# Kernel optimization log

Measured on AMD Instinct MI355X. Metric: run time of the kernel, lower is better.

Reference implementation:

```python
import jax, jax.numpy as jnp
import numpy as np

B, S, H = 16, 2048, 1024

def setup_inputs() -> dict:
    key = jax.random.key(0)
    ks = jax.random.split(key, 6)
    return {
        "h": jax.random.normal(ks[0], (1, B, H), jnp.float32),
        "c": jax.random.normal(ks[1], (1, B, H), jnp.float32),
        "encoder_outputs": jax.random.normal(ks[2], (B, S, H), jnp.float32),
        "attn_W": jax.random.normal(ks[3], (H, 2 * H), jnp.float32) * 0.02,
        "attn_b": jax.random.normal(ks[4], (H,), jnp.float32) * 0.02,
        "v_W": jax.random.normal(ks[5], (1, H), jnp.float32) * 0.02,
    }

def reference(h, c, encoder_outputs, attn_W, attn_b, v_W):
    # h: (1,B,H) -> (B,1,H); a: (B,S,H)
    a = encoder_outputs
    hq = jnp.transpose(h, (1, 0, 2))  # (B,1,H)
    # cat((s, a), -1) @ attn_W.T == s @ Wh.T + a @ Wa.T (avoids (B,S,2H) buffer)
    Wh, Wa = attn_W[:, :H], attn_W[:, H:]
    energy = jax.nn.relu(
        jnp.einsum("bqh,oh->bqo", hq, Wh)          # (B,1,H), broadcast over S
        + jnp.einsum("bsh,oh->bso", a, Wa)
        + attn_b
    )  # (B,S,H)
    scores = jnp.einsum("bsh,h->bs", energy, v_W[0])  # (B,S)
    attn_weights = jax.nn.softmax(scores, axis=1)      # (B,S)
    context = jnp.einsum("bs,bsh->bh", attn_weights, a)[:, None, :]  # (B,1,H)
    return context, attn_weights
```

## Files before the change

kernel.cpp:

```cpp
#include <hip/hip_runtime.h>
#include <hip/hip_bf16.h>


typedef __bf16 bf16x8 __attribute__((ext_vector_type(8)));
typedef float floatx4 __attribute__((ext_vector_type(4)));

#define BB 16
#define SS 2048
#define HH 1024
#define MM (BB * SS)

#define GLB(p) ((const __attribute__((address_space(1))) void*)(p))
#define LDSP(p) ((__attribute__((address_space(3))) void*)(p))

__device__ inline ushort f2bf(float x) {
    uint32_t u = __builtin_bit_cast(uint32_t, x);
    u += 0x7FFFu + ((u >> 16) & 1u);
    return (ushort)(u >> 16);
}

__global__ __launch_bounds__(256) void prep_all_kernel(
    const float* __restrict__ h, const float* __restrict__ W,
    const float* __restrict__ bias,
    float* __restrict__ projh, __bf16* __restrict__ Wb,
    float* __restrict__ sp0, float* __restrict__ ctx)
{
    int bid = blockIdx.x;
    int tid = threadIdx.x;
    if (bid < 256) {
        int b = bid >> 4;
        int oc = bid & 15;
        __shared__ float hrow[HH];
        *(float4*)&hrow[tid * 4] = *(const float4*)(h + (size_t)b * HH + tid * 4);
        __syncthreads();
        int ol = tid >> 2;
        int kq = tid & 3;
        int o = oc * 64 + ol;
        const float* wr = W + (size_t)o * (2 * HH) + kq * 256;
        const float* hb = hrow + kq * 256;
        float sum = 0.f;
        for (int k = 0; k < 256; k += 4) {
            float4 wv = *(const float4*)(wr + k);
            sum += hb[k] * wv.x + hb[k + 1] * wv.y + hb[k + 2] * wv.z + hb[k + 3] * wv.w;
        }
        sum += __shfl_xor(sum, 1);
        sum += __shfl_xor(sum, 2);
        if (kq == 0) projh[b * HH + o] = sum + bias[o];
    } else if (bid < 320) {
        int cb = bid - 256;
#pragma unroll
        for (int j = 0; j < 8; j++) {
            int g = cb * 2048 + tid + j * 256;
            int o = g >> 7;
            int k = (g & 127) * 8;
            const float* s = W + (size_t)o * (2 * HH) + HH + k;
            float4 x = *(const float4*)(s);
            float4 y = *(const float4*)(s + 4);
            union { ushort u[8]; uint4 v; } p;
            p.u[0] = f2bf(x.x); p.u[1] = f2bf(x.y); p.u[2] = f2bf(x.z); p.u[3] = f2bf(x.w);
            p.u[4] = f2bf(y.x); p.u[5] = f2bf(y.y); p.u[6] = f2bf(y.z); p.u[7] = f2bf(y.w);
            *(uint4*)(Wb + (size_t)o * HH + k) = p.v;
        }
    } else {
        int zb = bid - 320;
        float4 z = make_float4(0.f, 0.f, 0.f, 0.f);
        float* sp = sp0 + zb * 2048 + tid * 8;
        *(float4*)(sp) = z;
        *(float4*)(sp + 4) = z;
        *(float4*)(ctx + zb * 1024 + tid * 4) = z;
    }
}

__global__ __launch_bounds__(512, 2) void gemm_scores_kernel(
    const float* __restrict__ Af,
    const __bf16* __restrict__ Wb,
    const float* __restrict__ projh,
    const float* __restrict__ vW,
    float* __restrict__ scores_part)
{
    __shared__ __align__(16) char smem_raw[147456];
    __bf16* sB = (__bf16*)(smem_raw + 98304);

    const int bid = blockIdx.x;
    const int m0 = (((bid >> 5) << 3) + (bid & 7)) * 256;
    const int nq = (bid >> 3) & 3;
    const int n0 = nq * 256;
    const int bidx = m0 >> 11;

    const int tid = threadIdx.x;
    const int lane = tid & 63;
    const int wave = tid >> 6;
    const int wm = (wave & 1) * 128;
    const int wn = (wave >> 1) * 64;
    const int quad = lane >> 4;
    const int l16 = lane & 15;

    floatx4 acc[8][4];
    const floatx4 z = {0.f, 0.f, 0.f, 0.f};
#pragma unroll
    for (int i = 0; i < 8; i++)
#pragma unroll
        for (int j = 0; j < 4; j++) acc[i][j] = z;

    const int rb = lane >> 3;
    const int cchunk = ((lane & 7) ^ rb) * 4;
    const float* gAq0 = Af + (size_t)(m0 +   0 + wave * 8 + rb) * HH + cchunk;
    const float* gAq1 = Af + (size_t)(m0 +  64 + wave * 8 + rb) * HH + cchunk;
    const float* gAq2 = Af + (size_t)(m0 + 128 + wave * 8 + rb) * HH + cchunk;
    const float* gAq3 = Af + (size_t)(m0 + 192 + wave * 8 + rb) * HH + cchunk;

    const int su = tid >> 3;
    const int sj = (tid & 7) ^ (su & 7);
    const int g_row = su * 2 + (sj >> 2);
    const int g_col = (sj & 3) * 8;
    const __bf16* gB0 = Wb + (size_t)(n0 + g_row) * HH + g_col;
    const __bf16* gB1 = gB0 + (size_t)128 * HH;

    const int axL = (quad * 32) ^ ((l16 & 7) << 4);
    const int axH = axL ^ 16;
    int arow[8];
#pragma unroll
    for (int i = 0; i < 8; i++) arow[i] = (wm + i * 16 + l16) * 128;

    int boff[4];
#pragma unroll
    for (int j = 0; j < 4; j++) {
        int frow = wn + j * 16 + l16;
        int r7 = frow & 127;
        int u2 = r7 >> 1;
        int cc = u2 * 8 + (((((r7 & 1) << 2) | quad)) ^ (u2 & 7));
        boff[j] = (frow >> 7) * 4096 + cc * 8;
    }

#define STAGE_A(S, KF)                                                                       \
    {                                                                                        \
        char* dA_ = smem_raw + (S) * 32768 + wave * 1024;                                    \
        __builtin_amdgcn_global_load_lds(GLB(gAq0 + (KF)), LDSP(dA_), 16, 0, 0);             \
        __builtin_amdgcn_global_load_lds(GLB(gAq1 + (KF)), LDSP(dA_ + 8192), 16, 0, 0);      \
        __builtin_amdgcn_global_load_lds(GLB(gAq2 + (KF)), LDSP(dA_ + 16384), 16, 0, 0);     \
        __builtin_amdgcn_global_load_lds(GLB(gAq3 + (KF)), LDSP(dA_ + 24576), 16, 0, 0);     \
    }
#define STAGE_B(S, KF)                                                                       \
    {                                                                                        \
        __bf16* dB_ = sB + (S) * 8192 + wave * 512;                                          \
        __builtin_amdgcn_global_load_lds(GLB(gB0 + (KF)), LDSP(dB_), 16, 0, 0);              \
        __builtin_amdgcn_global_load_lds(GLB(gB1 + (KF)), LDSP(dB_ + 4096), 16, 0, 0);       \
    }
#define CVT8(dst, L, H)                                                     \
    {                                                                       \
        dst[0] = (__bf16)(L).x; dst[1] = (__bf16)(L).y;                     \
        dst[2] = (__bf16)(L).z; dst[3] = (__bf16)(L).w;                     \
        dst[4] = (__bf16)(H).x; dst[5] = (__bf16)(H).y;                     \
        dst[6] = (__bf16)(H).z; dst[7] = (__bf16)(H).w;                     \
    }
#define MFMA_LO                                                                            \
    _Pragma("unroll") for (int i_ = 0; i_ < 4; i_++)                                       \
        _Pragma("unroll") for (int j_ = 0; j_ < 4; j_++)                                   \
            acc[i_][j_] = __builtin_amdgcn_mfma_f32_16x16x32_bf16(af[i_], bfr[j_], acc[i_][j_], 0, 0, 0);
#define MFMA_HI                                                                            \
    _Pragma("unroll") for (int i_ = 0; i_ < 4; i_++)                                       \
        _Pragma("unroll") for (int j_ = 0; j_ < 4; j_++)                                   \
            acc[i_ + 4][j_] = __builtin_amdgcn_mfma_f32_16x16x32_bf16(af2[i_], bfr[j_], acc[i_ + 4][j_], 0, 0, 0);
#define BAR __builtin_amdgcn_s_barrier()
#define LGKM0 asm volatile("s_waitcnt lgkmcnt(0)" ::: "memory")
#define VM6 asm volatile("s_waitcnt vmcnt(6)" ::: "memory")
#define VM0 asm volatile("s_waitcnt vmcnt(0)" ::: "memory")
#define NOPW
#define PRIO1 __builtin_amdgcn_s_setprio(1)
#define PRIO0 __builtin_amdgcn_s_setprio(0)

#define KTILE(SC, SN, KF, DOST, VMW_)                                        \
    {                                                                        \
        const char* ab_ = smem_raw + (SC) * 32768;                           \
        const __bf16* bb_ = sB + (SC) * 8192;                                \
                                                                \
        bfr[0] = *(const bf16x8*)(bb_ + boff[0]);                            \
        bfr[1] = *(const bf16x8*)(bb_ + boff[1]);                            \
        bfr[2] = *(const bf16x8*)(bb_ + boff[2]);                            \
        bfr[3] = *(const bf16x8*)(bb_ + boff[3]);                            \
        floatx4 aL0 = *(const floatx4*)(ab_ + arow[0] + axL);                \
        floatx4 aH0 = *(const floatx4*)(ab_ + arow[0] + axH);                \
        floatx4 aL1 = *(const floatx4*)(ab_ + arow[1] + axL);                \
        floatx4 aH1 = *(const floatx4*)(ab_ + arow[1] + axH);                \
        floatx4 aL2 = *(const floatx4*)(ab_ + arow[2] + axL);                \
        floatx4 aH2 = *(const floatx4*)(ab_ + arow[2] + axH);                \
        floatx4 aL3 = *(const floatx4*)(ab_ + arow[3] + axL);                \
        floatx4 aH3 = *(const floatx4*)(ab_ + arow[3] + axH);                \
        if (DOST) STAGE_A(SN, KF);                                           \
        BAR; LGKM0;                                                          \
        CVT8(af[0], aL0, aH0); CVT8(af[1], aL1, aH1);                        \
        CVT8(af[2], aL2, aH2); CVT8(af[3], aL3, aH3);                        \
        PRIO1; MFMA_LO; PRIO0; BAR;                                          \
                                                                \
        floatx4 cL0 = *(const floatx4*)(ab_ + arow[4] + axL);                \
        floatx4 cH0 = *(const floatx4*)(ab_ + arow[4] + axH);                \
        floatx4 cL1 = *(const floatx4*)(ab_ + arow[5] + axL);                \
        floatx4 cH1 = *(const floatx4*)(ab_ + arow[5] + axH);                \
        floatx4 cL2 = *(const floatx4*)(ab_ + arow[6] + axL);                \
        floatx4 cH2 = *(const floatx4*)(ab_ + arow[6] + axH);                \
        floatx4 cL3 = *(const floatx4*)(ab_ + arow[7] + axL);                \
        floatx4 cH3 = *(const floatx4*)(ab_ + arow[7] + axH);                \
        if (DOST) STAGE_B(SN, KF);                                           \
        VMW_;                                                                \
        BAR; LGKM0;                                                          \
        CVT8(af2[0], cL0, cH0); CVT8(af2[1], cL1, cH1);                      \
        CVT8(af2[2], cL2, cH2); CVT8(af2[3], cL3, cH3);                      \
        PRIO1; MFMA_HI; PRIO0; BAR;                                          \
    }

    bf16x8 af[4], af2[4], bfr[4];

    STAGE_A(0, 0);
    STAGE_B(0, 0);
    STAGE_A(1, 32);
    STAGE_B(1, 32);
    VM6;
    BAR;

    for (int g = 0; g < 10; ++g) {
        const int kf0 = (3 * g + 2) * 32;
        KTILE(0, 2, kf0, 1, VM6)
        KTILE(1, 0, kf0 + 32, 1, VM6)
        KTILE(2, 1, kf0 + 64, 1, VM6)
    }
    KTILE(0, 2, 0, 0, VM0)
    KTILE(1, 0, 0, 0, NOPW)

#undef KTILE
#undef STAGE_A
#undef STAGE_B
#undef CVT8
#undef MFMA_LO
#undef MFMA_HI
#undef BAR
#undef LGKM0
#undef VM6
#undef VM0
#undef NOPW
#undef PRIO1
#undef PRIO0

    float ph[4], vv[4];
#pragma unroll
    for (int j = 0; j < 4; j++) {
        int ng = n0 + wn + j * 16 + l16;
        ph[j] = projh[bidx * HH + ng];
        vv[j] = vW[ng];
    }

    float* red = (float*)smem_raw;
    __syncthreads();
    if (tid < 256) red[tid] = 0.f;
    __syncthreads();

#pragma unroll
    for (int i = 0; i < 8; i++) {
        float s[4] = {0.f, 0.f, 0.f, 0.f};
#pragma unroll
        for (int j = 0; j < 4; j++) {
#pragma unroll
            for (int r2 = 0; r2 < 4; r2++) {
                float e = acc[i][j][r2] + ph[j];
                e = e > 0.f ? e : 0.f;
                s[r2] += e * vv[j];
            }
        }
#pragma unroll
        for (int r2 = 0; r2 < 4; r2++) {
            s[r2] += __shfl_xor(s[r2], 1);
            s[r2] += __shfl_xor(s[r2], 2);
            s[r2] += __shfl_xor(s[r2], 4);
            s[r2] += __shfl_xor(s[r2], 8);
        }
        if (l16 == 0) {
#pragma unroll
            for (int r2 = 0; r2 < 4; r2++)
                atomicAdd(&red[wm + i * 16 + quad * 4 + r2], s[r2]);
        }
    }
    __syncthreads();
    if (tid < 256) scores_part[(size_t)nq * MM + m0 + tid] = red[tid];
}

__global__ __launch_bounds__(256) void gemm_scores_f32_kernel(
    const float* __restrict__ A, const float* __restrict__ W,
    const float* __restrict__ projh, const float* __restrict__ vW,
    float* __restrict__ scores)
{
    constexpr int BM = 128, BN = 128, BK = 32, LDT = BK + 8;
    __shared__ __bf16 As[BM * LDT];
    __shared__ __bf16 Bs[BN * LDT];
    const int n0 = blockIdx.x * BN;
    const int m0 = blockIdx.y * BM;
    const int bidx = m0 >> 11;
    const int tid = threadIdx.x;
    const int lane = tid & 63;
    const int wave = tid >> 6;
    const int wm = (wave & 1) * 64;
    const int wn = (wave >> 1) * 64;
    const int quad = lane >> 4;
    const int l16 = lane & 15;
    floatx4 acc[4][4];
    const floatx4 z = {0.f, 0.f, 0.f, 0.f};
#pragma unroll
    for (int i = 0; i < 4; i++)
#pragma unroll
        for (int j = 0; j < 4; j++) acc[i][j] = z;
    int rowT[4], colT[4];
#pragma unroll
    for (int i = 0; i < 4; i++) {
        int fi = tid + 256 * i;
        rowT[i] = fi >> 3;
        colT[i] = (fi & 7) * 4;
    }
    for (int k0 = 0; k0 < HH; k0 += BK) {
        float4 av[4], bv[4];
#pragma unroll
        for (int i = 0; i < 4; i++) {
            av[i] = *(const float4*)(A + (size_t)(m0 + rowT[i]) * HH + k0 + colT[i]);
            bv[i] = *(const float4*)(W + (size_t)(n0 + rowT[i]) * (2 * HH) + HH + k0 + colT[i]);
        }
        __syncthreads();
#pragma unroll
        for (int i = 0; i < 4; i++) {
            ushort4 ua = make_ushort4(f2bf(av[i].x), f2bf(av[i].y), f2bf(av[i].z), f2bf(av[i].w));
            ushort4 ub = make_ushort4(f2bf(bv[i].x), f2bf(bv[i].y), f2bf(bv[i].z), f2bf(bv[i].w));
            *(ushort4*)&As[rowT[i] * LDT + colT[i]] = ua;
            *(ushort4*)&Bs[rowT[i] * LDT + colT[i]] = ub;
        }
        __syncthreads();
        bf16x8 af[4], bf[4];
#pragma unroll
        for (int i = 0; i < 4; i++)
            af[i] = *(const bf16x8*)&As[(wm + i * 16 + l16) * LDT + quad * 8];
#pragma unroll
        for (int j = 0; j < 4; j++)
            bf[j] = *(const bf16x8*)&Bs[(wn + j * 16 + l16) * LDT + quad * 8];
#pragma unroll
        for (int i = 0; i < 4; i++)
#pragma unroll
            for (int j = 0; j < 4; j++)
                acc[i][j] = __builtin_amdgcn_mfma_f32_16x16x32_bf16(af[i], bf[j], acc[i][j], 0, 0, 0);
    }
    float ph[4], vv[4];
#pragma unroll
    for (int j = 0; j < 4; j++) {
        int ng = n0 + wn + j * 16 + l16;
        ph[j] = projh[bidx * HH + ng];
        vv[j] = vW[ng];
    }
#pragma unroll
    for (int i = 0; i < 4; i++) {
        float s[4] = {0.f, 0.f, 0.f, 0.f};
#pragma unroll
        for (int j = 0; j < 4; j++) {
#pragma unroll
            for (int r = 0; r < 4; r++) {
                float e = acc[i][j][r] + ph[j];
                e = e > 0.f ? e : 0.f;
                s[r] += e * vv[j];
            }
        }
#pragma unroll
        for (int r = 0; r < 4; r++) {
            s[r] += __shfl_xor(s[r], 1);
            s[r] += __shfl_xor(s[r], 2);
            s[r] += __shfl_xor(s[r], 4);
            s[r] += __shfl_xor(s[r], 8);
        }
        if (l16 == 0) {
#pragma unroll
            for (int r = 0; r < 4; r++) {
                int mg = m0 + wm + i * 16 + quad * 4 + r;
                atomicAdd(&scores[mg], s[r]);
            }
        }
    }
}

__global__ __launch_bounds__(256) void softmax_context_kernel(
    const float* __restrict__ A, const float* __restrict__ scores_part,
    int nparts, float* __restrict__ wout, float* __restrict__ ctx)
{
    int b = blockIdx.x >> 5;
    int sc = blockIdx.x & 31;
    int tid = threadIdx.x;
    const float* srow = scores_part + b * SS;

    float x[8];
    float mx = -1e30f;
#pragma unroll
    for (int i = 0; i < 8; i++) {
        int idx = tid + i * 256;
        float v = srow[idx];
        for (int q = 1; q < nparts; q++) v += srow[(size_t)q * MM + idx];
        x[i] = v; mx = fmaxf(mx, v);
    }
#pragma unroll
    for (int off = 32; off; off >>= 1) mx = fmaxf(mx, __shfl_xor(mx, off));
    __shared__ float redm[4], reds[4];
    if ((tid & 63) == 0) redm[tid >> 6] = mx;
    __syncthreads();
    mx = fmaxf(fmaxf(redm[0], redm[1]), fmaxf(redm[2], redm[3]));
    float sum = 0.f;
#pragma unroll
    for (int i = 0; i < 8; i++) sum += __expf(x[i] - mx);
#pragma unroll
    for (int off = 32; off; off >>= 1) sum += __shfl_xor(sum, off);
    if ((tid & 63) == 0) reds[tid >> 6] = sum;
    __syncthreads();
    float inv = 1.0f / (reds[0] + reds[1] + reds[2] + reds[3]);

    __shared__ float wsm[64];
    if (tid < 64) {
        int idx = sc * 64 + tid;
        float v = srow[idx];
        for (int q = 1; q < nparts; q++) v += srow[(size_t)q * MM + idx];
        float wv = __expf(v - mx) * inv;
        wsm[tid] = wv;
        wout[b * SS + idx] = wv;
    }
    __syncthreads();

    const float* arow = A + ((size_t)b * SS + sc * 64) * HH + tid * 4;
    float4 acc = make_float4(0.f, 0.f, 0.f, 0.f);
#pragma unroll 4
    for (int s = 0; s < 64; s++) {
        float w = wsm[s];
        float4 v = *(const float4*)(arow + (size_t)s * HH);
        acc.x += w * v.x; acc.y += w * v.y; acc.z += w * v.z; acc.w += w * v.w;
    }
    float* o = ctx + b * HH + tid * 4;
    atomicAdd(o + 0, acc.x);
    atomicAdd(o + 1, acc.y);
    atomicAdd(o + 2, acc.z);
    atomicAdd(o + 3, acc.w);
}

extern "C" void kernel_launch(void* const* d_in, const int* in_sizes, int n_in,
                              void* d_out, int out_size, void* d_ws, size_t ws_size,
                              hipStream_t stream) {
    const float* h    = (const float*)d_in[0];
    const float* a    = (const float*)d_in[2];
    const float* W    = (const float*)d_in[3];
    const float* bias = (const float*)d_in[4];
    const float* vW   = (const float*)d_in[5];
    float* out = (float*)d_out;

    float* projh       = (float*)d_ws;
    float* scores_part = projh + BB * HH;
    __bf16* Wb = (__bf16*)(scores_part + 4 * MM);
    const size_t need = (size_t)(BB * HH + 4 * MM) * 4 + (size_t)HH * HH * 2;

    if (ws_size >= need) {
        prep_all_kernel<<<336, 256, 0, stream>>>(h, W, bias, projh, Wb, scores_part, out);
        gemm_scores_kernel<<<512, 512, 0, stream>>>(a, Wb, projh, vW, scores_part);
        softmax_context_kernel<<<BB * 32, 256, 0, stream>>>(
            a, scores_part, 4, out + BB * HH, out);
    } else {
        prep_all_kernel<<<336, 256, 0, stream>>>(h, W, bias, projh, Wb, scores_part, out);
        gemm_scores_f32_kernel<<<dim3(HH / 128, MM / 128), 256, 0, stream>>>(
            a, W, projh, vW, scores_part);
        softmax_context_kernel<<<BB * 32, 256, 0, stream>>>(
            a, scores_part, 1, out + BB * HH, out);
    }
}
```

Measured before the change: 288.0 us.

## Retile score GEMM to 256x512 blocks with 1024 threads and double buffering

Switches the fused score GEMM from 512 blocks of 512 threads (256x256 tiles, three-stage LDS pipeline) to 256 blocks of 1024 threads, each computing a 256x512 tile with a simple two-stage double buffer. Each block now covers half of N instead of a quarter, so the fp32 encoder activations are loaded from global memory twice rather than four times, and the score partials drop from four to two. The price is a shallower pipeline with a full vmcnt(0) wait and barrier every k-step, half as many blocks, and higher register pressure from 32 accumulators per wave under launch_bounds(1024,4).

```diff
diff --git a/kernel.cpp b/kernel.cpp
--- a/kernel.cpp
+++ b/kernel.cpp
@@ -71,60 +71,58 @@
     }
 }
 
-__global__ __launch_bounds__(512, 2) void gemm_scores_kernel(
+__global__ __launch_bounds__(1024, 4) void gemm_scores_kernel(
     const float* __restrict__ Af,
     const __bf16* __restrict__ Wb,
     const float* __restrict__ projh,
     const float* __restrict__ vW,
     float* __restrict__ scores_part)
 {
-    __shared__ __align__(16) char smem_raw[147456];
-    __bf16* sB = (__bf16*)(smem_raw + 98304);
+    __shared__ __align__(16) char smem_raw[131072];
 
     const int bid = blockIdx.x;
-    const int m0 = (((bid >> 5) << 3) + (bid & 7)) * 256;
-    const int nq = (bid >> 3) & 3;
-    const int n0 = nq * 256;
+    const int g = ((bid & 7) << 5) | (bid >> 3);
+    const int nq = g & 1;
+    const int m0 = (g >> 1) * 256;
+    const int n0 = nq * 512;
     const int bidx = m0 >> 11;
 
     const int tid = threadIdx.x;
     const int lane = tid & 63;
     const int wave = tid >> 6;
-    const int wm = (wave & 1) * 128;
-    const int wn = (wave >> 1) * 64;
+    const int wm = (wave >> 2) * 64;
+    const int wn = (wave & 3) * 128;
     const int quad = lane >> 4;
     const int l16 = lane & 15;
 
-    floatx4 acc[8][4];
+    floatx4 acc[4][8];
     const floatx4 z = {0.f, 0.f, 0.f, 0.f};
 #pragma unroll
-    for (int i = 0; i < 8; i++)
-#pragma unroll
-        for (int j = 0; j < 4; j++) acc[i][j] = z;
+    for (int i = 0; i < 4; i++)
+#pragma unroll
+        for (int j = 0; j < 8; j++) acc[i][j] = z;
 
     const int rb = lane >> 3;
-    const int cchunk = ((lane & 7) ^ rb) * 4;
-    const float* gAq0 = Af + (size_t)(m0 +   0 + wave * 8 + rb) * HH + cchunk;
-    const float* gAq1 = Af + (size_t)(m0 +  64 + wave * 8 + rb) * HH + cchunk;
-    const float* gAq2 = Af + (size_t)(m0 + 128 + wave * 8 + rb) * HH + cchunk;
-    const float* gAq3 = Af + (size_t)(m0 + 192 + wave * 8 + rb) * HH + cchunk;
+    const int cch = ((lane & 7) ^ rb) * 4;
+    const float* gA0 = Af + (size_t)(m0 + wave * 8 + rb) * HH + cch;
+    const float* gA1 = gA0 + (size_t)128 * HH;
 
     const int su = tid >> 3;
     const int sj = (tid & 7) ^ (su & 7);
     const int g_row = su * 2 + (sj >> 2);
     const int g_col = (sj & 3) * 8;
     const __bf16* gB0 = Wb + (size_t)(n0 + g_row) * HH + g_col;
-    const __bf16* gB1 = gB0 + (size_t)128 * HH;
+    const __bf16* gB1 = gB0 + (size_t)256 * HH;
 
     const int axL = (quad * 32) ^ ((l16 & 7) << 4);
     const int axH = axL ^ 16;
-    int arow[8];
-#pragma unroll
-    for (int i = 0; i < 8; i++) arow[i] = (wm + i * 16 + l16) * 128;
-
-    int boff[4];
-#pragma unroll
-    for (int j = 0; j < 4; j++) {
+    int arow[4];
+#pragma unroll
+    for (int i = 0; i < 4; i++) arow[i] = (wm + i * 16 + l16) * 128;
+
+    int boff[8];
+#pragma unroll
+    for (int j = 0; j < 8; j++) {
         int frow = wn + j * 16 + l16;
         int r7 = frow & 127;
         int u2 = r7 >> 1;
@@ -132,19 +130,17 @@
         boff[j] = (frow >> 7) * 4096 + cc * 8;
     }
 
-#define STAGE_A(S, KF)                                                                       \
-    {                                                                                        \
-        char* dA_ = smem_raw + (S) * 32768 + wave * 1024;                                    \
-        __builtin_amdgcn_global_load_lds(GLB(gAq0 + (KF)), LDSP(dA_), 16, 0, 0);             \
-        __builtin_amdgcn_global_load_lds(GLB(gAq1 + (KF)), LDSP(dA_ + 8192), 16, 0, 0);      \
-        __builtin_amdgcn_global_load_lds(GLB(gAq2 + (KF)), LDSP(dA_ + 16384), 16, 0, 0);     \
-        __builtin_amdgcn_global_load_lds(GLB(gAq3 + (KF)), LDSP(dA_ + 24576), 16, 0, 0);     \
-    }
-#define STAGE_B(S, KF)                                                                       \
-    {                                                                                        \
-        __bf16* dB_ = sB + (S) * 8192 + wave * 512;                                          \
-        __builtin_amdgcn_global_load_lds(GLB(gB0 + (KF)), LDSP(dB_), 16, 0, 0);              \
-        __builtin_amdgcn_global_load_lds(GLB(gB1 + (KF)), LDSP(dB_ + 4096), 16, 0, 0);       \
+#define STAGE_A(S, KF)                                                                        \
+    {                                                                                         \
+        char* dA_ = smem_raw + (S) * 32768 + wave * 1024;                                     \
+        __builtin_amdgcn_global_load_lds(GLB(gA0 + (KF)), LDSP(dA_), 16, 0, 0);               \
+        __builtin_amdgcn_global_load_lds(GLB(gA1 + (KF)), LDSP(dA_ + 16384), 16, 0, 0);       \
+    }
+#define STAGE_B(S, KF)                                                                        \
+    {                                                                                         \
+        char* dB_ = smem_raw + 65536 + (S) * 32768 + wave * 1024;                             \
+        __builtin_amdgcn_global_load_lds(GLB(gB0 + (KF)), LDSP(dB_), 16, 0, 0);               \
+        __builtin_amdgcn_global_load_lds(GLB(gB1 + (KF)), LDSP(dB_ + 16384), 16, 0, 0);       \
     }
 #define CVT8(dst, L, H)                                                     \
     {                                                                       \
@@ -153,96 +149,61 @@
         dst[4] = (__bf16)(H).x; dst[5] = (__bf16)(H).y;                     \
         dst[6] = (__bf16)(H).z; dst[7] = (__bf16)(H).w;                     \
     }
-#define MFMA_LO                                                                            \
-    _Pragma("unroll") for (int i_ = 0; i_ < 4; i_++)                                       \
-        _Pragma("unroll") for (int j_ = 0; j_ < 4; j_++)                                   \
-            acc[i_][j_] = __builtin_amdgcn_mfma_f32_16x16x32_bf16(af[i_], bfr[j_], acc[i_][j_], 0, 0, 0);
-#define MFMA_HI                                                                            \
-    _Pragma("unroll") for (int i_ = 0; i_ < 4; i_++)                                       \
-        _Pragma("unroll") for (int j_ = 0; j_ < 4; j_++)                                   \
-            acc[i_ + 4][j_] = __builtin_amdgcn_mfma_f32_16x16x32_bf16(af2[i_], bfr[j_], acc[i_ + 4][j_], 0, 0, 0);
 #define BAR __builtin_amdgcn_s_barrier()
-#define LGKM0 asm volatile("s_waitcnt lgkmcnt(0)" ::: "memory")
-#define VM6 asm volatile("s_waitcnt vmcnt(6)" ::: "memory")
 #define VM0 asm volatile("s_waitcnt vmcnt(0)" ::: "memory")
-#define NOPW
 #define PRIO1 __builtin_amdgcn_s_setprio(1)
 #define PRIO0 __builtin_amdgcn_s_setprio(0)
 
-#define KTILE(SC, SN, KF, DOST, VMW_)                                        \
-    {                                                                        \
-        const char* ab_ = smem_raw + (SC) * 32768;                           \
-        const __bf16* bb_ = sB + (SC) * 8192;                                \
-                                                                \
-        bfr[0] = *(const bf16x8*)(bb_ + boff[0]);                            \
-        bfr[1] = *(const bf16x8*)(bb_ + boff[1]);                            \
-        bfr[2] = *(const bf16x8*)(bb_ + boff[2]);                            \
-        bfr[3] = *(const bf16x8*)(bb_ + boff[3]);                            \
-        floatx4 aL0 = *(const floatx4*)(ab_ + arow[0] + axL);                \
-        floatx4 aH0 = *(const floatx4*)(ab_ + arow[0] + axH);                \
-        floatx4 aL1 = *(const floatx4*)(ab_ + arow[1] + axL);                \
-        floatx4 aH1 = *(const floatx4*)(ab_ + arow[1] + axH);                \
-        floatx4 aL2 = *(const floatx4*)(ab_ + arow[2] + axL);                \
-        floatx4 aH2 = *(const floatx4*)(ab_ + arow[2] + axH);                \
-        floatx4 aL3 = *(const floatx4*)(ab_ + arow[3] + axL);                \
-        floatx4 aH3 = *(const floatx4*)(ab_ + arow[3] + axH);                \
-        if (DOST) STAGE_A(SN, KF);                                           \
-        BAR; LGKM0;                                                          \
-        CVT8(af[0], aL0, aH0); CVT8(af[1], aL1, aH1);                        \
-        CVT8(af[2], aL2, aH2); CVT8(af[3], aL3, aH3);                        \
-        PRIO1; MFMA_LO; PRIO0; BAR;                                          \
-                                                                \
-        floatx4 cL0 = *(const floatx4*)(ab_ + arow[4] + axL);                \
-        floatx4 cH0 = *(const floatx4*)(ab_ + arow[4] + axH);                \
-        floatx4 cL1 = *(const floatx4*)(ab_ + arow[5] + axL);                \
-        floatx4 cH1 = *(const floatx4*)(ab_ + arow[5] + axH);                \
-        floatx4 cL2 = *(const floatx4*)(ab_ + arow[6] + axL);                \
-        floatx4 cH2 = *(const floatx4*)(ab_ + arow[6] + axH);                \
-        floatx4 cL3 = *(const floatx4*)(ab_ + arow[7] + axL);                \
-        floatx4 cH3 = *(const floatx4*)(ab_ + arow[7] + axH);                \
-        if (DOST) STAGE_B(SN, KF);                                           \
-        VMW_;                                                                \
-        BAR; LGKM0;                                                          \
-        CVT8(af2[0], cL0, cH0); CVT8(af2[1], cL1, cH1);                      \
-        CVT8(af2[2], cL2, cH2); CVT8(af2[3], cL3, cH3);                      \
-        PRIO1; MFMA_HI; PRIO0; BAR;                                          \
-    }
-
-    bf16x8 af[4], af2[4], bfr[4];
-
     STAGE_A(0, 0);
     STAGE_B(0, 0);
-    STAGE_A(1, 32);
-    STAGE_B(1, 32);
-    VM6;
+    VM0;
     BAR;
 
-    for (int g = 0; g < 10; ++g) {
-        const int kf0 = (3 * g + 2) * 32;
-        KTILE(0, 2, kf0, 1, VM6)
-        KTILE(1, 0, kf0 + 32, 1, VM6)
-        KTILE(2, 1, kf0 + 64, 1, VM6)
-    }
-    KTILE(0, 2, 0, 0, VM0)
-    KTILE(1, 0, 0, 0, NOPW)
-
-#undef KTILE
+#pragma unroll 2
+    for (int kt = 0; kt < 32; ++kt) {
+        const int cur = kt & 1;
+        if (kt < 31) {
+            const int kf = (kt + 1) * 32;
+            STAGE_A(cur ^ 1, kf);
+            STAGE_B(cur ^ 1, kf);
+        }
+        const char* ab = smem_raw + cur * 32768;
+        const __bf16* bb = (const __bf16*)(smem_raw + 65536) + cur * 16384;
+
+        bf16x8 bf[8];
+#pragma unroll
+        for (int j = 0; j < 8; j++) bf[j] = *(const bf16x8*)(bb + boff[j]);
+
+        PRIO1;
+#pragma unroll
+        for (int i = 0; i < 4; i++) {
+            floatx4 aL = *(const floatx4*)(ab + arow[i] + axL);
+            floatx4 aH = *(const floatx4*)(ab + arow[i] + axH);
+            bf16x8 af;
+            CVT8(af, aL, aH);
+#pragma unroll
+            for (int j = 0; j < 8; j++)
+                acc[i][j] = __builtin_amdgcn_mfma_f32_16x16x32_bf16(af, bf[j], acc[i][j], 0, 0, 0);
+        }
+        PRIO0;
+
+        if (kt < 31) {
+            VM0;
+            BAR;
+        }
+    }
+
 #undef STAGE_A
 #undef STAGE_B
 #undef CVT8
-#undef MFMA_LO
-#undef MFMA_HI
 #undef BAR
-#undef LGKM0
-#undef VM6
 #undef VM0
-#undef NOPW
 #undef PRIO1
 #undef PRIO0
 
-    float ph[4], vv[4];
-#pragma unroll
-    for (int j = 0; j < 4; j++) {
+    float ph[8], vv[8];
+#pragma unroll
+    for (int j = 0; j < 8; j++) {
         int ng = n0 + wn + j * 16 + l16;
         ph[j] = projh[bidx * HH + ng];
         vv[j] = vW[ng];
@@ -254,10 +215,10 @@
     __syncthreads();
 
 #pragma unroll
-    for (int i = 0; i < 8; i++) {
+    for (int i = 0; i < 4; i++) {
         float s[4] = {0.f, 0.f, 0.f, 0.f};
 #pragma unroll
-        for (int j = 0; j < 4; j++) {
+        for (int j = 0; j < 8; j++) {
 #pragma unroll
             for (int r2 = 0; r2 < 4; r2++) {
                 float e = acc[i][j][r2] + ph[j];
@@ -454,9 +415,9 @@
 
     if (ws_size >= need) {
         prep_all_kernel<<<336, 256, 0, stream>>>(h, W, bias, projh, Wb, scores_part, out);
-        gemm_scores_kernel<<<512, 512, 0, stream>>>(a, Wb, projh, vW, scores_part);
+        gemm_scores_kernel<<<256, 1024, 0, stream>>>(a, Wb, projh, vW, scores_part);
         softmax_context_kernel<<<BB * 32, 256, 0, stream>>>(
-            a, scores_part, 4, out + BB * HH, out);
+            a, scores_part, 2, out + BB * HH, out);
     } else {
         prep_all_kernel<<<336, 256, 0, stream>>>(h, W, bias, projh, Wb, scores_part, out);
         gemm_scores_f32_kernel<<<dim3(HH / 128, MM / 128), 256, 0, stream>>>(
```

Measured after the change: 838.0 us. +191.0%, slower.
